# Optimization experiments

Hardware: AMD Instinct MI355X
Metric: run time of the kernel (lower is better)

## Reference

```python
import jax, jax.numpy as jnp
import numpy as np

DIM = 1024
NUM_HEADS = 16
HEAD_DIM = DIM // NUM_HEADS
SCALE = HEAD_DIM ** -0.5
CAUSAL = True


def setup_inputs() -> dict:
    key = jax.random.key(0)
    k_x, k_qkv, k_proj, k_pb = jax.random.split(key, 4)
    B, S = 4, 2048
    x = jax.random.normal(k_x, (B, S, DIM), dtype=jnp.float32)
    # nn.Linear(dim, 3*dim, bias=False): weight [3*dim, dim]; store transposed [dim, 3*dim]
    w_qkv = jax.random.normal(k_qkv, (DIM, 3 * DIM), dtype=jnp.float32) * (DIM ** -0.5)
    w_proj = jax.random.normal(k_proj, (DIM, DIM), dtype=jnp.float32) * (DIM ** -0.5)
    b_proj = jax.random.normal(k_pb, (DIM,), dtype=jnp.float32) * 0.01
    return {"x": x, "w_qkv": w_qkv, "w_proj": w_proj, "b_proj": b_proj}


def reference(x, w_qkv, w_proj, b_proj):
    B, S, C = x.shape
    # qkv: [B, S, 3, H, D] -> q,k,v each [B, H, S, D]
    qkv = (x @ w_qkv).reshape(B, S, 3, NUM_HEADS, HEAD_DIM)
    qkv = jnp.transpose(qkv, (2, 0, 3, 1, 4))
    q, k, v = qkv[0], qkv[1], qkv[2]
    # scores [B, H, S, S]
    attn = jnp.einsum('bhqd,bhkd->bhqk', q, k) * SCALE
    if CAUSAL:
        causal_mask = jnp.triu(jnp.ones((S, S), dtype=bool), k=1)
        attn = jnp.where(causal_mask, -jnp.inf, attn)
    attn = jax.nn.softmax(attn, axis=-1)
    out = jnp.einsum('bhqk,bhkd->bhqd', attn, v)
    out = jnp.transpose(out, (0, 2, 1, 3)).reshape(B, S, C)
    return out @ w_proj + b_proj
```

## Files before the change

### kernel.cpp

```cpp
#include <hip/hip_runtime.h>
#include <hip/hip_bf16.h>
#include <math.h>

#define DIMC 1024
#define NHEADS 16
#define HDIM 64
#define BATCH 4
#define SEQ 2048
#define NROWS (BATCH * SEQ)
#define ATTN_SCALE 0.125f
#define LOG2E 1.4426950408889634f

typedef __attribute__((ext_vector_type(8))) short short8;
typedef __attribute__((ext_vector_type(4))) short short4v;
typedef __attribute__((ext_vector_type(4))) float f32x4;

static __device__ __forceinline__ short f2bf(float f) {
    __hip_bfloat16 h = __float2bfloat16(f);
    return *reinterpret_cast<short*>(&h);
}

static __device__ __forceinline__ void gload16(const void* g, void* l) {
    __builtin_amdgcn_global_load_lds(
        (const __attribute__((address_space(1))) unsigned int*)g,
        (__attribute__((address_space(3))) unsigned int*)l, 16, 0, 0);
}

__global__ __launch_bounds__(256)
void xcvt(const float* __restrict__ in, unsigned short* __restrict__ out) {
    int i = blockIdx.x * 256 + threadIdx.x;
    const float4* p = reinterpret_cast<const float4*>(in) + 2 * i;
    float4 a = p[0], b = p[1];
    short8 pk;
    pk[0] = f2bf(a.x); pk[1] = f2bf(a.y); pk[2] = f2bf(a.z); pk[3] = f2bf(a.w);
    pk[4] = f2bf(b.x); pk[5] = f2bf(b.y); pk[6] = f2bf(b.z); pk[7] = f2bf(b.w);
    reinterpret_cast<short8*>(out)[i] = pk;
}

__global__ __launch_bounds__(256)
void transpose_cvt(const float* __restrict__ src, unsigned short* __restrict__ dst,
                   int N) {
    __shared__ float t[64][65];
    const int tid = threadIdx.x;
    const int cb = blockIdx.x * 64;
    const int rb = blockIdx.y * 64;
#pragma unroll
    for (int e = 0; e < 4; e++) {
        int idx = tid + e * 256;
        int row = idx >> 4;
        int c4 = (idx & 15) << 2;
        *reinterpret_cast<float4*>(&t[row][c4]) =
            *reinterpret_cast<const float4*>(&src[(size_t)(rb + row) * N + cb + c4]);
    }
    __syncthreads();
#pragma unroll
    for (int e = 0; e < 2; e++) {
        int idx = tid + e * 256;
        int col = idx >> 3;
        int k8 = (idx & 7) << 3;
        short8 pk;
#pragma unroll
        for (int j = 0; j < 8; j++) pk[j] = f2bf(t[k8 + j][col]);
        *reinterpret_cast<short8*>(&dst[(size_t)(cb + col) * 1024 + rb + k8]) = pk;
    }
}

__global__ __launch_bounds__(256)
void qkv_gemm_mfma(const unsigned short* __restrict__ Xbf,
                   const unsigned short* __restrict__ Wt,
                   unsigned short* __restrict__ qo, unsigned short* __restrict__ ko,
                   unsigned short* __restrict__ vt) {
    __shared__ short Alds[128][64];
    __shared__ short Blds[128][64];
    const int tid = threadIdx.x;
    const int lane = tid & 63;
    const int wave = tid >> 6;
    const int wr = wave >> 1, wc = wave & 1;
    const int rowbase = blockIdx.y * 128;
    const int colbase = blockIdx.x * 128;
    const int g = lane >> 4, li = lane & 15;
    const int sr = lane >> 3;
    const int sc = (lane & 7) * 8;
    short* aflat = &Alds[0][0];
    short* bflat = &Blds[0][0];

    f32x4 acc[4][4];
#pragma unroll
    for (int m = 0; m < 4; m++)
#pragma unroll
        for (int n = 0; n < 4; n++) acc[m][n] = (f32x4){0.f, 0.f, 0.f, 0.f};

    for (int k0 = 0; k0 < DIMC; k0 += 64) {
#pragma unroll
        for (int e = 0; e < 4; e++) {
            int j = wave * 4 + e;
            gload16(&Xbf[(size_t)(rowbase + j * 8 + sr) * DIMC + k0 + sc],
                    aflat + j * 512);
            gload16(&Wt[(size_t)(colbase + j * 8 + sr) * 1024 + k0 + sc],
                    bflat + j * 512);
        }
        __syncthreads();
#pragma unroll
        for (int ks = 0; ks < 2; ks++) {
            short8 af[4], bfr[4];
#pragma unroll
            for (int m = 0; m < 4; m++)
                af[m] = *reinterpret_cast<const short8*>(
                    &Alds[wr * 64 + m * 16 + li][ks * 32 + g * 8]);
#pragma unroll
            for (int n = 0; n < 4; n++)
                bfr[n] = *reinterpret_cast<const short8*>(
                    &Blds[wc * 64 + n * 16 + li][ks * 32 + g * 8]);
#pragma unroll
            for (int m = 0; m < 4; m++)
#pragma unroll
                for (int n = 0; n < 4; n++)
                    acc[m][n] = __builtin_amdgcn_mfma_f32_16x16x32_bf16(
                        af[m], bfr[n], acc[m][n], 0, 0, 0);
        }
        __syncthreads();
    }

    const int col0 = colbase + wc * 64;
    const int three = col0 >> 10;
    const int h = (col0 & 1023) >> 6;
    if (three < 2) {
        unsigned short* dst = (three == 0) ? qo : ko;
        const float mult = (three == 0) ? (ATTN_SCALE * LOG2E) : 1.0f;
#pragma unroll
        for (int n = 0; n < 4; n++) {
            int d = n * 16 + li;
#pragma unroll
            for (int m = 0; m < 4; m++) {
                int r0 = rowbase + wr * 64 + m * 16 + g * 4;
                int b = r0 >> 11;
                size_t base = ((size_t)(b * NHEADS + h) * SEQ) * HDIM + d;
#pragma unroll
                for (int r = 0; r < 4; r++) {
                    int s = (r0 + r) & 2047;
                    dst[base + (size_t)s * HDIM] = (unsigned short)f2bf(acc[m][n][r] * mult);
                }
            }
        }
    } else {
#pragma unroll
        for (int n = 0; n < 4; n++) {
            int d = n * 16 + li;
#pragma unroll
            for (int m = 0; m < 4; m++) {
                int r0 = rowbase + wr * 64 + m * 16 + g * 4;
                int b = r0 >> 11, s0 = r0 & 2047;
                short4v pk;
#pragma unroll
                for (int r = 0; r < 4; r++) pk[r] = f2bf(acc[m][n][r]);
                *reinterpret_cast<short4v*>(
                    &vt[((size_t)(b * NHEADS + h) * HDIM + d) * SEQ + s0]) = pk;
            }
        }
    }
}

__global__ __launch_bounds__(256)
void proj_gemm_mfma(const unsigned short* __restrict__ Abf,
                    const unsigned short* __restrict__ Wt,
                    const float* __restrict__ bias, float* __restrict__ out) {
    __shared__ short Alds[128][64];
    __shared__ short Blds[128][64];
    const int tid = threadIdx.x;
    const int lane = tid & 63;
    const int wave = tid >> 6;
    const int wr = wave >> 1, wc = wave & 1;
    const int rowbase = blockIdx.y * 128;
    const int colbase = blockIdx.x * 128;
    const int g = lane >> 4, li = lane & 15;
    const int sr = lane >> 3;
    const int sc = (lane & 7) * 8;
    short* aflat = &Alds[0][0];
    short* bflat = &Blds[0][0];

    f32x4 acc[4][4];
#pragma unroll
    for (int m = 0; m < 4; m++)
#pragma unroll
        for (int n = 0; n < 4; n++) acc[m][n] = (f32x4){0.f, 0.f, 0.f, 0.f};

    for (int k0 = 0; k0 < DIMC; k0 += 64) {
#pragma unroll
        for (int e = 0; e < 4; e++) {
            int j = wave * 4 + e;
            gload16(&Abf[(size_t)(rowbase + j * 8 + sr) * DIMC + k0 + sc],
                    aflat + j * 512);
            gload16(&Wt[(size_t)(colbase + j * 8 + sr) * 1024 + k0 + sc],
                    bflat + j * 512);
        }
        __syncthreads();
#pragma unroll
        for (int ks = 0; ks < 2; ks++) {
            short8 af[4], bfr[4];
#pragma unroll
            for (int m = 0; m < 4; m++)
                af[m] = *reinterpret_cast<const short8*>(
                    &Alds[wr * 64 + m * 16 + li][ks * 32 + g * 8]);
#pragma unroll
            for (int n = 0; n < 4; n++)
                bfr[n] = *reinterpret_cast<const short8*>(
                    &Blds[wc * 64 + n * 16 + li][ks * 32 + g * 8]);
#pragma unroll
            for (int m = 0; m < 4; m++)
#pragma unroll
                for (int n = 0; n < 4; n++)
                    acc[m][n] = __builtin_amdgcn_mfma_f32_16x16x32_bf16(
                        af[m], bfr[n], acc[m][n], 0, 0, 0);
        }
        __syncthreads();
    }

#pragma unroll
    for (int n = 0; n < 4; n++) {
        int col = colbase + wc * 64 + n * 16 + li;
        float bv = bias[col];
#pragma unroll
        for (int m = 0; m < 4; m++) {
            int r0 = rowbase + wr * 64 + m * 16 + g * 4;
#pragma unroll
            for (int r = 0; r < 4; r++)
                out[(size_t)(r0 + r) * DIMC + col] = acc[m][n][r] + bv;
        }
    }
}

__global__ __launch_bounds__(256)
void flash_attn_mfma(const unsigned short* __restrict__ qg,
                     const unsigned short* __restrict__ kg,
                     const unsigned short* __restrict__ vt,
                     unsigned short* __restrict__ og) {
    __shared__ short Klds[2][64][64];
    __shared__ short Vlds[2][64][64];
    __shared__ short Plds[4][32][64];
    const int tid = threadIdx.x;
    const int lane = tid & 63;
    const int w = tid >> 6;
    const int g = lane >> 4, li = lane & 15;
    const int sw = li & 7;
    const int orig = blockIdx.x;
    const int swz = (orig & 7) * 64 + (orig >> 3);
    const int bx = swz & 7;
    const int bh = swz >> 3;
    const size_t head = (size_t)bh * SEQ * HDIM;
    const int b = bh >> 4, h = bh & 15;

    const int c0r = tid >> 3, c0c = tid & 7;

    for (int pass = 0; pass < 2; pass++) {
        const int qtile = pass ? (15 - bx) : bx;
        const int qbase = qtile * 128;
        const int qw = qbase + w * 32;
        const int nt = 2 * qtile + 2;

        short8 bq[2][2];
#pragma unroll
        for (int n = 0; n < 2; n++)
#pragma unroll
            for (int ds = 0; ds < 2; ds++)
                bq[n][ds] = *reinterpret_cast<const short8*>(
                    &qg[head + (size_t)(qw + li + 16 * n) * HDIM + ds * 32 + g * 8]);

        f32x4 accO[4][2];
#pragma unroll
        for (int df = 0; df < 4; df++)
#pragma unroll
            for (int n = 0; n < 2; n++) accO[df][n] = (f32x4){0.f, 0.f, 0.f, 0.f};
        float mrow[2] = {-INFINITY, -INFINITY};
        float lrow[2] = {0.f, 0.f};

        const unsigned short* kp = kg + head + (size_t)c0r * HDIM + c0c * 8;
        const unsigned short* vp = vt + head + (size_t)c0r * SEQ + c0c * 8;

        short8 kreg0, kreg1, vreg0, vreg1;
        kreg0 = *reinterpret_cast<const short8*>(kp);
        kreg1 = *reinterpret_cast<const short8*>(kp + 32 * HDIM);
        vreg0 = *reinterpret_cast<const short8*>(vp);
        vreg1 = *reinterpret_cast<const short8*>(vp + 32 * SEQ);
        kp += 64 * HDIM; vp += 64;
        {
            const int sw0 = (c0c ^ (c0r & 7)) * 8;
            const int sw1 = (c0c ^ ((c0r + 32) & 7)) * 8;
            *reinterpret_cast<short8*>(&Klds[0][c0r][sw0]) = kreg0;
            *reinterpret_cast<short8*>(&Vlds[0][c0r][sw0]) = vreg0;
            *reinterpret_cast<short8*>(&Klds[0][c0r + 32][sw1]) = kreg1;
            *reinterpret_cast<short8*>(&Vlds[0][c0r + 32][sw1]) = vreg1;
        }
        __syncthreads();

        for (int t = 0; t < nt; t++) {
            const int kvbase = t * 64;
            const int buf = t & 1;
            const bool more = (t + 1 < nt);
            if (more) {
                kreg0 = *reinterpret_cast<const short8*>(kp);
                kreg1 = *reinterpret_cast<const short8*>(kp + 32 * HDIM);
                vreg0 = *reinterpret_cast<const short8*>(vp);
                vreg1 = *reinterpret_cast<const short8*>(vp + 32 * SEQ);
                kp += 64 * HDIM; vp += 64;
            }

            if (kvbase <= qw + 31) {
                f32x4 s[4][2];
#pragma unroll
                for (int m = 0; m < 4; m++)
#pragma unroll
                    for (int n = 0; n < 2; n++) s[m][n] = (f32x4){0.f, 0.f, 0.f, 0.f};
#pragma unroll
                for (int ds = 0; ds < 2; ds++) {
                    short8 ak[4];
#pragma unroll
                    for (int m = 0; m < 4; m++)
                        ak[m] = *reinterpret_cast<const short8*>(
                            &Klds[buf][li + 16 * m][(((ds * 4 + g) ^ sw)) * 8]);
#pragma unroll
                    for (int m = 0; m < 4; m++)
#pragma unroll
                        for (int n = 0; n < 2; n++)
                            s[m][n] = __builtin_amdgcn_mfma_f32_16x16x32_bf16(
                                ak[m], bq[n][ds], s[m][n], 0, 0, 0);
                }
                const bool diag = (kvbase + 63 > qw);
                if (diag) {
#pragma unroll
                    for (int n = 0; n < 2; n++) {
                        int q = qw + li + 16 * n;
#pragma unroll
                        for (int m = 0; m < 4; m++)
#pragma unroll
                            for (int r = 0; r < 4; r++) {
                                int kv = kvbase + 16 * m + 4 * g + r;
                                if (kv > q) s[m][n][r] = -INFINITY;
                            }
                    }
                }
                float corr[2];
#pragma unroll
                for (int n = 0; n < 2; n++) {
                    float a0 = fmaxf(fmaxf(s[0][n][0], s[0][n][1]), fmaxf(s[0][n][2], s[0][n][3]));
                    float a1 = fmaxf(fmaxf(s[1][n][0], s[1][n][1]), fmaxf(s[1][n][2], s[1][n][3]));
                    float a2 = fmaxf(fmaxf(s[2][n][0], s[2][n][1]), fmaxf(s[2][n][2], s[2][n][3]));
                    float a3 = fmaxf(fmaxf(s[3][n][0], s[3][n][1]), fmaxf(s[3][n][2], s[3][n][3]));
                    float tm = fmaxf(fmaxf(a0, a1), fmaxf(a2, a3));
                    tm = fmaxf(tm, __shfl_xor(tm, 16));
                    tm = fmaxf(tm, __shfl_xor(tm, 32));
                    float mnew = fmaxf(mrow[n], tm);
                    corr[n] = __builtin_amdgcn_exp2f(mrow[n] - mnew);
                    mrow[n] = mnew;
                }
                float sm[4][2];
#pragma unroll
                for (int m = 0; m < 4; m++) {
#pragma unroll
                    for (int n = 0; n < 2; n++) {
                        float p0 = __builtin_amdgcn_exp2f(s[m][n][0] - mrow[n]);
                        float p1 = __builtin_amdgcn_exp2f(s[m][n][1] - mrow[n]);
                        float p2 = __builtin_amdgcn_exp2f(s[m][n][2] - mrow[n]);
                        float p3 = __builtin_amdgcn_exp2f(s[m][n][3] - mrow[n]);
                        sm[m][n] = (p0 + p1) + (p2 + p3);
                        unsigned u01 = (__float_as_uint(p1) & 0xFFFF0000u) |
                                       (__float_as_uint(p0) >> 16);
                        unsigned u23 = (__float_as_uint(p3) & 0xFFFF0000u) |
                                       (__float_as_uint(p2) >> 16);
                        *reinterpret_cast<uint2*>(
                            &Plds[w][li + 16 * n]
                                 [((2 * m + (g >> 1)) ^ sw) * 8 + (g & 1) * 4]) =
                            make_uint2(u01, u23);
                    }
                }
#pragma unroll
                for (int n = 0; n < 2; n++) {
                    float ts = (sm[0][n] + sm[1][n]) + (sm[2][n] + sm[3][n]);
                    ts += __shfl_xor(ts, 16);
                    ts += __shfl_xor(ts, 32);
                    lrow[n] = lrow[n] * corr[n] + ts;
                }
                bool nore = (corr[0] == 1.0f) && (corr[1] == 1.0f);
                if (!__all((int)nore)) {
#pragma unroll
                    for (int df = 0; df < 4; df++)
#pragma unroll
                        for (int n = 0; n < 2; n++) {
                            accO[df][n][0] *= corr[n]; accO[df][n][1] *= corr[n];
                            accO[df][n][2] *= corr[n]; accO[df][n][3] *= corr[n];
                        }
                }
#pragma unroll
                for (int ks = 0; ks < 2; ks++) {
                    short8 av[4], bp[2];
#pragma unroll
                    for (int df = 0; df < 4; df++)
                        av[df] = *reinterpret_cast<const short8*>(
                            &Vlds[buf][li + 16 * df][((ks * 4 + g) ^ sw) * 8]);
#pragma unroll
                    for (int n = 0; n < 2; n++)
                        bp[n] = *reinterpret_cast<const short8*>(
                            &Plds[w][li + 16 * n][((ks * 4 + g) ^ sw) * 8]);
#pragma unroll
                    for (int df = 0; df < 4; df++)
#pragma unroll
                        for (int n = 0; n < 2; n++)
                            accO[df][n] = __builtin_amdgcn_mfma_f32_16x16x32_bf16(
                                av[df], bp[n], accO[df][n], 0, 0, 0);
                }
            }

            if (more) {
                const int nbuf = buf ^ 1;
                const int sw0 = (c0c ^ (c0r & 7)) * 8;
                const int sw1 = (c0c ^ ((c0r + 32) & 7)) * 8;
                *reinterpret_cast<short8*>(&Klds[nbuf][c0r][sw0]) = kreg0;
                *reinterpret_cast<short8*>(&Vlds[nbuf][c0r][sw0]) = vreg0;
                *reinterpret_cast<short8*>(&Klds[nbuf][c0r + 32][sw1]) = kreg1;
                *reinterpret_cast<short8*>(&Vlds[nbuf][c0r + 32][sw1]) = vreg1;
            }
            __syncthreads();
        }

#pragma unroll
        for (int n = 0; n < 2; n++) {
            float inv = 1.0f / lrow[n];
            int q = qw + li + 16 * n;
            size_t rowoff = (size_t)(b * SEQ + q) * DIMC + h * HDIM;
#pragma unroll
            for (int df = 0; df < 4; df++) {
                short4v pk;
#pragma unroll
                for (int r = 0; r < 4; r++) pk[r] = f2bf(accO[df][n][r] * inv);
                *reinterpret_cast<short4v*>(&og[rowoff + 16 * df + 4 * g]) = pk;
            }
        }
        __syncthreads();
    }
}

extern "C" void kernel_launch(void* const* d_in, const int* in_sizes, int n_in,
                              void* d_out, int out_size, void* d_ws, size_t ws_size,
                              hipStream_t stream) {
    const float* x      = (const float*)d_in[0];
    const float* w_qkv  = (const float*)d_in[1];
    const float* w_proj = (const float*)d_in[2];
    const float* b_proj = (const float*)d_in[3];
    float* out = (float*)d_out;

    char* w = (char*)d_ws;
    unsigned short* qb  = (unsigned short*)(w);
    unsigned short* kb  = (unsigned short*)(w + ((size_t)16 << 20));
    unsigned short* vtb = (unsigned short*)(w + ((size_t)32 << 20));
    unsigned short* ao  = (unsigned short*)(w + ((size_t)48 << 20));
    unsigned short* wqt = (unsigned short*)(w + ((size_t)64 << 20));
    unsigned short* wpt = (unsigned short*)(w + ((size_t)72 << 20));
    unsigned short* xbf = (unsigned short*)(w + ((size_t)80 << 20));

    xcvt<<<NROWS * DIMC / (256 * 8), 256, 0, stream>>>(x, xbf);
    transpose_cvt<<<dim3(3 * DIMC / 64, DIMC / 64), 256, 0, stream>>>(w_qkv, wqt, 3 * DIMC);
    transpose_cvt<<<dim3(DIMC / 64, DIMC / 64), 256, 0, stream>>>(w_proj, wpt, DIMC);
    qkv_gemm_mfma<<<dim3(3 * DIMC / 128, NROWS / 128), 256, 0, stream>>>(xbf, wqt, qb, kb, vtb);
    flash_attn_mfma<<<512, 256, 0, stream>>>(qb, kb, vtb, ao);
    proj_gemm_mfma<<<dim3(DIMC / 128, NROWS / 128), 256, 0, stream>>>(ao, wpt, b_proj, out);
}
```

Measured before the change: 279.7 us.

## Swizzle GEMM LDS tiles and split flash attention across eight waves

The two GEMM kernels now XOR-swizzle the column chunk used when staging A/B tiles into LDS and when reading MFMA fragments, so fragment reads hit fewer LDS bank conflicts. The flash attention kernel moves from 256 to 512 threads per block, with each wave owning 16 query rows instead of 32. Each thread then loads one K/V chunk per tile instead of two, and per-wave register state (accumulators, running max and sum) is halved. In exchange, each wave reuses every K/V fragment read from LDS for half as many rows, and a larger block needs more waves resident per CU.

```diff
diff --git a/kernel.cpp b/kernel.cpp
--- a/kernel.cpp
+++ b/kernel.cpp
@@ -80,7 +80,8 @@
     const int colbase = blockIdx.x * 128;
     const int g = lane >> 4, li = lane & 15;
     const int sr = lane >> 3;
-    const int sc = (lane & 7) * 8;
+    const int sc = ((lane & 7) ^ sr) * 8;
+    const int swk = li & 7;
     short* aflat = &Alds[0][0];
     short* bflat = &Blds[0][0];
 
@@ -106,11 +107,11 @@
 #pragma unroll
             for (int m = 0; m < 4; m++)
                 af[m] = *reinterpret_cast<const short8*>(
-                    &Alds[wr * 64 + m * 16 + li][ks * 32 + g * 8]);
+                    &Alds[wr * 64 + m * 16 + li][((ks * 4 + g) ^ swk) * 8]);
 #pragma unroll
             for (int n = 0; n < 4; n++)
                 bfr[n] = *reinterpret_cast<const short8*>(
-                    &Blds[wc * 64 + n * 16 + li][ks * 32 + g * 8]);
+                    &Blds[wc * 64 + n * 16 + li][((ks * 4 + g) ^ swk) * 8]);
 #pragma unroll
             for (int m = 0; m < 4; m++)
 #pragma unroll
@@ -174,7 +175,8 @@
     const int colbase = blockIdx.x * 128;
     const int g = lane >> 4, li = lane & 15;
     const int sr = lane >> 3;
-    const int sc = (lane & 7) * 8;
+    const int sc = ((lane & 7) ^ sr) * 8;
+    const int swk = li & 7;
     short* aflat = &Alds[0][0];
     short* bflat = &Blds[0][0];
 
@@ -200,11 +202,11 @@
 #pragma unroll
             for (int m = 0; m < 4; m++)
                 af[m] = *reinterpret_cast<const short8*>(
-                    &Alds[wr * 64 + m * 16 + li][ks * 32 + g * 8]);
+                    &Alds[wr * 64 + m * 16 + li][((ks * 4 + g) ^ swk) * 8]);
 #pragma unroll
             for (int n = 0; n < 4; n++)
                 bfr[n] = *reinterpret_cast<const short8*>(
-                    &Blds[wc * 64 + n * 16 + li][ks * 32 + g * 8]);
+                    &Blds[wc * 64 + n * 16 + li][((ks * 4 + g) ^ swk) * 8]);
 #pragma unroll
             for (int m = 0; m < 4; m++)
 #pragma unroll
@@ -229,14 +231,14 @@
     }
 }
 
-__global__ __launch_bounds__(256)
+__global__ __launch_bounds__(512)
 void flash_attn_mfma(const unsigned short* __restrict__ qg,
                      const unsigned short* __restrict__ kg,
                      const unsigned short* __restrict__ vt,
                      unsigned short* __restrict__ og) {
     __shared__ short Klds[2][64][64];
     __shared__ short Vlds[2][64][64];
-    __shared__ short Plds[4][32][64];
+    __shared__ short Plds[8][16][64];
     const int tid = threadIdx.x;
     const int lane = tid & 63;
     const int w = tid >> 6;
@@ -254,41 +256,32 @@
     for (int pass = 0; pass < 2; pass++) {
         const int qtile = pass ? (15 - bx) : bx;
         const int qbase = qtile * 128;
-        const int qw = qbase + w * 32;
+        const int qw = qbase + w * 16;
         const int nt = 2 * qtile + 2;
 
-        short8 bq[2][2];
-#pragma unroll
-        for (int n = 0; n < 2; n++)
-#pragma unroll
-            for (int ds = 0; ds < 2; ds++)
-                bq[n][ds] = *reinterpret_cast<const short8*>(
-                    &qg[head + (size_t)(qw + li + 16 * n) * HDIM + ds * 32 + g * 8]);
-
-        f32x4 accO[4][2];
-#pragma unroll
-        for (int df = 0; df < 4; df++)
-#pragma unroll
-            for (int n = 0; n < 2; n++) accO[df][n] = (f32x4){0.f, 0.f, 0.f, 0.f};
-        float mrow[2] = {-INFINITY, -INFINITY};
-        float lrow[2] = {0.f, 0.f};
+        short8 bq[2];
+#pragma unroll
+        for (int ds = 0; ds < 2; ds++)
+            bq[ds] = *reinterpret_cast<const short8*>(
+                &qg[head + (size_t)(qw + li) * HDIM + ds * 32 + g * 8]);
+
+        f32x4 accO[4];
+#pragma unroll
+        for (int df = 0; df < 4; df++) accO[df] = (f32x4){0.f, 0.f, 0.f, 0.f};
+        float mrow = -INFINITY;
+        float lrow = 0.f;
 
         const unsigned short* kp = kg + head + (size_t)c0r * HDIM + c0c * 8;
         const unsigned short* vp = vt + head + (size_t)c0r * SEQ + c0c * 8;
 
-        short8 kreg0, kreg1, vreg0, vreg1;
-        kreg0 = *reinterpret_cast<const short8*>(kp);
-        kreg1 = *reinterpret_cast<const short8*>(kp + 32 * HDIM);
-        vreg0 = *reinterpret_cast<const short8*>(vp);
-        vreg1 = *reinterpret_cast<const short8*>(vp + 32 * SEQ);
+        short8 kreg, vreg;
+        kreg = *reinterpret_cast<const short8*>(kp);
+        vreg = *reinterpret_cast<const short8*>(vp);
         kp += 64 * HDIM; vp += 64;
         {
             const int sw0 = (c0c ^ (c0r & 7)) * 8;
-            const int sw1 = (c0c ^ ((c0r + 32) & 7)) * 8;
-            *reinterpret_cast<short8*>(&Klds[0][c0r][sw0]) = kreg0;
-            *reinterpret_cast<short8*>(&Vlds[0][c0r][sw0]) = vreg0;
-            *reinterpret_cast<short8*>(&Klds[0][c0r + 32][sw1]) = kreg1;
-            *reinterpret_cast<short8*>(&Vlds[0][c0r + 32][sw1]) = vreg1;
+            *reinterpret_cast<short8*>(&Klds[0][c0r][sw0]) = kreg;
+            *reinterpret_cast<short8*>(&Vlds[0][c0r][sw0]) = vreg;
         }
         __syncthreads();
 
@@ -297,140 +290,109 @@
             const int buf = t & 1;
             const bool more = (t + 1 < nt);
             if (more) {
-                kreg0 = *reinterpret_cast<const short8*>(kp);
-                kreg1 = *reinterpret_cast<const short8*>(kp + 32 * HDIM);
-                vreg0 = *reinterpret_cast<const short8*>(vp);
-                vreg1 = *reinterpret_cast<const short8*>(vp + 32 * SEQ);
+                kreg = *reinterpret_cast<const short8*>(kp);
+                vreg = *reinterpret_cast<const short8*>(vp);
                 kp += 64 * HDIM; vp += 64;
             }
 
-            if (kvbase <= qw + 31) {
-                f32x4 s[4][2];
-#pragma unroll
-                for (int m = 0; m < 4; m++)
-#pragma unroll
-                    for (int n = 0; n < 2; n++) s[m][n] = (f32x4){0.f, 0.f, 0.f, 0.f};
+            if (kvbase <= qw + 15) {
+                f32x4 s[4];
+#pragma unroll
+                for (int m = 0; m < 4; m++) s[m] = (f32x4){0.f, 0.f, 0.f, 0.f};
 #pragma unroll
                 for (int ds = 0; ds < 2; ds++) {
                     short8 ak[4];
 #pragma unroll
                     for (int m = 0; m < 4; m++)
                         ak[m] = *reinterpret_cast<const short8*>(
-                            &Klds[buf][li + 16 * m][(((ds * 4 + g) ^ sw)) * 8]);
+                            &Klds[buf][li + 16 * m][((ds * 4 + g) ^ sw) * 8]);
 #pragma unroll
                     for (int m = 0; m < 4; m++)
-#pragma unroll
-                        for (int n = 0; n < 2; n++)
-                            s[m][n] = __builtin_amdgcn_mfma_f32_16x16x32_bf16(
-                                ak[m], bq[n][ds], s[m][n], 0, 0, 0);
+                        s[m] = __builtin_amdgcn_mfma_f32_16x16x32_bf16(
+                            ak[m], bq[ds], s[m], 0, 0, 0);
                 }
                 const bool diag = (kvbase + 63 > qw);
                 if (diag) {
-#pragma unroll
-                    for (int n = 0; n < 2; n++) {
-                        int q = qw + li + 16 * n;
-#pragma unroll
-                        for (int m = 0; m < 4; m++)
-#pragma unroll
-                            for (int r = 0; r < 4; r++) {
-                                int kv = kvbase + 16 * m + 4 * g + r;
-                                if (kv > q) s[m][n][r] = -INFINITY;
-                            }
+                    int q = qw + li;
+#pragma unroll
+                    for (int m = 0; m < 4; m++)
+#pragma unroll
+                        for (int r = 0; r < 4; r++) {
+                            int kv = kvbase + 16 * m + 4 * g + r;
+                            if (kv > q) s[m][r] = -INFINITY;
+                        }
+                }
+                float a0 = fmaxf(fmaxf(s[0][0], s[0][1]), fmaxf(s[0][2], s[0][3]));
+                float a1 = fmaxf(fmaxf(s[1][0], s[1][1]), fmaxf(s[1][2], s[1][3]));
+                float a2 = fmaxf(fmaxf(s[2][0], s[2][1]), fmaxf(s[2][2], s[2][3]));
+                float a3 = fmaxf(fmaxf(s[3][0], s[3][1]), fmaxf(s[3][2], s[3][3]));
+                float tm = fmaxf(fmaxf(a0, a1), fmaxf(a2, a3));
+                tm = fmaxf(tm, __shfl_xor(tm, 16));
+                tm = fmaxf(tm, __shfl_xor(tm, 32));
+                float mnew = fmaxf(mrow, tm);
+                float corr = __builtin_amdgcn_exp2f(mrow - mnew);
+                mrow = mnew;
+                float sm[4];
+#pragma unroll
+                for (int m = 0; m < 4; m++) {
+                    float p0 = __builtin_amdgcn_exp2f(s[m][0] - mrow);
+                    float p1 = __builtin_amdgcn_exp2f(s[m][1] - mrow);
+                    float p2 = __builtin_amdgcn_exp2f(s[m][2] - mrow);
+                    float p3 = __builtin_amdgcn_exp2f(s[m][3] - mrow);
+                    sm[m] = (p0 + p1) + (p2 + p3);
+                    unsigned u01 = (__float_as_uint(p1) & 0xFFFF0000u) |
+                                   (__float_as_uint(p0) >> 16);
+                    unsigned u23 = (__float_as_uint(p3) & 0xFFFF0000u) |
+                                   (__float_as_uint(p2) >> 16);
+                    *reinterpret_cast<uint2*>(
+                        &Plds[w][li][((2 * m + (g >> 1)) ^ sw) * 8 + (g & 1) * 4]) =
+                        make_uint2(u01, u23);
+                }
+                float ts = (sm[0] + sm[1]) + (sm[2] + sm[3]);
+                ts += __shfl_xor(ts, 16);
+                ts += __shfl_xor(ts, 32);
+                lrow = lrow * corr + ts;
+                if (!__all((int)(corr == 1.0f))) {
+#pragma unroll
+                    for (int df = 0; df < 4; df++) {
+                        accO[df][0] *= corr; accO[df][1] *= corr;
+                        accO[df][2] *= corr; accO[df][3] *= corr;
                     }
                 }
-                float corr[2];
-#pragma unroll
-                for (int n = 0; n < 2; n++) {
-                    float a0 = fmaxf(fmaxf(s[0][n][0], s[0][n][1]), fmaxf(s[0][n][2], s[0][n][3]));
-                    float a1 = fmaxf(fmaxf(s[1][n][0], s[1][n][1]), fmaxf(s[1][n][2], s[1][n][3]));
-                    float a2 = fmaxf(fmaxf(s[2][n][0], s[2][n][1]), fmaxf(s[2][n][2], s[2][n][3]));
-                    float a3 = fmaxf(fmaxf(s[3][n][0], s[3][n][1]), fmaxf(s[3][n][2], s[3][n][3]));
-                    float tm = fmaxf(fmaxf(a0, a1), fmaxf(a2, a3));
-                    tm = fmaxf(tm, __shfl_xor(tm, 16));
-                    tm = fmaxf(tm, __shfl_xor(tm, 32));
-                    float mnew = fmaxf(mrow[n], tm);
-                    corr[n] = __builtin_amdgcn_exp2f(mrow[n] - mnew);
-                    mrow[n] = mnew;
-                }
-                float sm[4][2];
-#pragma unroll
-                for (int m = 0; m < 4; m++) {
-#pragma unroll
-                    for (int n = 0; n < 2; n++) {
-                        float p0 = __builtin_amdgcn_exp2f(s[m][n][0] - mrow[n]);
-                        float p1 = __builtin_amdgcn_exp2f(s[m][n][1] - mrow[n]);
-                        float p2 = __builtin_amdgcn_exp2f(s[m][n][2] - mrow[n]);
-                        float p3 = __builtin_amdgcn_exp2f(s[m][n][3] - mrow[n]);
-                        sm[m][n] = (p0 + p1) + (p2 + p3);
-                        unsigned u01 = (__float_as_uint(p1) & 0xFFFF0000u) |
-                                       (__float_as_uint(p0) >> 16);
-                        unsigned u23 = (__float_as_uint(p3) & 0xFFFF0000u) |
-                                       (__float_as_uint(p2) >> 16);
-                        *reinterpret_cast<uint2*>(
-                            &Plds[w][li + 16 * n]
-                                 [((2 * m + (g >> 1)) ^ sw) * 8 + (g & 1) * 4]) =
-                            make_uint2(u01, u23);
-                    }
-                }
-#pragma unroll
-                for (int n = 0; n < 2; n++) {
-                    float ts = (sm[0][n] + sm[1][n]) + (sm[2][n] + sm[3][n]);
-                    ts += __shfl_xor(ts, 16);
-                    ts += __shfl_xor(ts, 32);
-                    lrow[n] = lrow[n] * corr[n] + ts;
-                }
-                bool nore = (corr[0] == 1.0f) && (corr[1] == 1.0f);
-                if (!__all((int)nore)) {
-#pragma unroll
-                    for (int df = 0; df < 4; df++)
-#pragma unroll
-                        for (int n = 0; n < 2; n++) {
-                            accO[df][n][0] *= corr[n]; accO[df][n][1] *= corr[n];
-                            accO[df][n][2] *= corr[n]; accO[df][n][3] *= corr[n];
-                        }
-                }
 #pragma unroll
                 for (int ks = 0; ks < 2; ks++) {
-                    short8 av[4], bp[2];
+                    short8 av[4];
 #pragma unroll
                     for (int df = 0; df < 4; df++)
                         av[df] = *reinterpret_cast<const short8*>(
                             &Vlds[buf][li + 16 * df][((ks * 4 + g) ^ sw) * 8]);
-#pragma unroll
-                    for (int n = 0; n < 2; n++)
-                        bp[n] = *reinterpret_cast<const short8*>(
-                            &Plds[w][li + 16 * n][((ks * 4 + g) ^ sw) * 8]);
+                    short8 bp = *reinterpret_cast<const short8*>(
+                        &Plds[w][li][((ks * 4 + g) ^ sw) * 8]);
 #pragma unroll
                     for (int df = 0; df < 4; df++)
-#pragma unroll
-                        for (int n = 0; n < 2; n++)
-                            accO[df][n] = __builtin_amdgcn_mfma_f32_16x16x32_bf16(
-                                av[df], bp[n], accO[df][n], 0, 0, 0);
+                        accO[df] = __builtin_amdgcn_mfma_f32_16x16x32_bf16(
+                            av[df], bp, accO[df], 0, 0, 0);
                 }
             }
 
             if (more) {
                 const int nbuf = buf ^ 1;
                 const int sw0 = (c0c ^ (c0r & 7)) * 8;
-                const int sw1 = (c0c ^ ((c0r + 32) & 7)) * 8;
-                *reinterpret_cast<short8*>(&Klds[nbuf][c0r][sw0]) = kreg0;
-                *reinterpret_cast<short8*>(&Vlds[nbuf][c0r][sw0]) = vreg0;
-                *reinterpret_cast<short8*>(&Klds[nbuf][c0r + 32][sw1]) = kreg1;
-                *reinterpret_cast<short8*>(&Vlds[nbuf][c0r + 32][sw1]) = vreg1;
+                *reinterpret_cast<short8*>(&Klds[nbuf][c0r][sw0]) = kreg;
+                *reinterpret_cast<short8*>(&Vlds[nbuf][c0r][sw0]) = vreg;
             }
             __syncthreads();
         }
 
-#pragma unroll
-        for (int n = 0; n < 2; n++) {
-            float inv = 1.0f / lrow[n];
-            int q = qw + li + 16 * n;
+        {
+            float inv = 1.0f / lrow;
+            int q = qw + li;
             size_t rowoff = (size_t)(b * SEQ + q) * DIMC + h * HDIM;
 #pragma unroll
             for (int df = 0; df < 4; df++) {
                 short4v pk;
 #pragma unroll
-                for (int r = 0; r < 4; r++) pk[r] = f2bf(accO[df][n][r] * inv);
+                for (int r = 0; r < 4; r++) pk[r] = f2bf(accO[df][r] * inv);
                 *reinterpret_cast<short4v*>(&og[rowoff + 16 * df + 4 * g]) = pk;
             }
         }
@@ -460,6 +422,6 @@
     transpose_cvt<<<dim3(3 * DIMC / 64, DIMC / 64), 256, 0, stream>>>(w_qkv, wqt, 3 * DIMC);
     transpose_cvt<<<dim3(DIMC / 64, DIMC / 64), 256, 0, stream>>>(w_proj, wpt, DIMC);
     qkv_gemm_mfma<<<dim3(3 * DIMC / 128, NROWS / 128), 256, 0, stream>>>(xbf, wqt, qb, kb, vtb);
-    flash_attn_mfma<<<512, 256, 0, stream>>>(qb, kb, vtb, ao);
+    flash_attn_mfma<<<512, 512, 0, stream>>>(qb, kb, vtb, ao);
     proj_gemm_mfma<<<dim3(DIMC / 128, NROWS / 128), 256, 0, stream>>>(ao, wpt, b_proj, out);
 }
```

Result: faster. 250.7 us (-10.4%).
